# Kernel tuning notes

Measured on AMD Instinct MI355X. Metric: run time of the kernel, lower is better.

## Reference

```python
import jax, jax.numpy as jnp
import numpy as np

N_M, N_D, E = 20000, 8000, 200000
F_IN, H, O = 384, 512, 256  # feature dim, hidden_channels, out_channels
H1 = O * 2                  # conv1 output channels = 512


def setup_inputs() -> dict:
    key = jax.random.key(0)
    ks = jax.random.split(key, 32)

    def w(k, shape):
        return jax.random.normal(k, shape, dtype=jnp.float32) * 0.02

    inp = {
        # node features
        "mirna_feat": jax.random.normal(ks[0], (N_M, F_IN), dtype=jnp.float32),
        "dis_feat": jax.random.normal(ks[1], (N_D, F_IN), dtype=jnp.float32),
        # node ids and edge list (miRNA -> disease); reverse edges are the flip
        "mirna_node_id": jnp.arange(N_M, dtype=jnp.int32),
        "dis_node_id": jnp.arange(N_D, dtype=jnp.int32),
        "edge_src": jax.random.randint(ks[2], (E,), 0, N_M, dtype=jnp.int32),
        "edge_dst": jax.random.randint(ks[3], (E,), 0, N_D, dtype=jnp.int32),
        # input projections + embeddings
        "Wm": w(ks[4], (F_IN, H)), "bm": jnp.zeros((H,), jnp.float32),
        "Wd": w(ks[5], (F_IN, H)), "bd": jnp.zeros((H,), jnp.float32),
        "mirna_emb": w(ks[6], (N_M, H)),
        "dis_emb": w(ks[7], (N_D, H)),
        # layer1 SAGEConv per edge type (md: miRNA->disease, dm: reverse)
        "W1_md_l": w(ks[8], (H, H1)), "b1_md": jnp.zeros((H1,), jnp.float32), "W1_md_r": w(ks[9], (H, H1)),
        "W1_dm_l": w(ks[10], (H, H1)), "b1_dm": jnp.zeros((H1,), jnp.float32), "W1_dm_r": w(ks[11], (H, H1)),
        # layer2 SAGEConv per edge type
        "W2_md_l": w(ks[12], (H1, O)), "b2_md": jnp.zeros((O,), jnp.float32), "W2_md_r": w(ks[13], (H1, O)),
        "W2_dm_l": w(ks[14], (H1, O)), "b2_dm": jnp.zeros((O,), jnp.float32), "W2_dm_r": w(ks[15], (H1, O)),
    }
    return inp


def _mean_agg(x_src, src_idx, dst_idx, n_dst):
    # gather src features per edge, segment-mean onto destinations (0 for isolated nodes)
    msg = jnp.take(x_src, src_idx, axis=0)               # [E, d]
    agg = jax.ops.segment_sum(msg, dst_idx, num_segments=n_dst)
    cnt = jax.ops.segment_sum(jnp.ones((dst_idx.shape[0],), x_src.dtype), dst_idx, num_segments=n_dst)
    return agg / jnp.maximum(cnt, 1.0)[:, None]


def _sage(x_src, x_dst, src_idx, dst_idx, Wl, bl, Wr):
    mean = _mean_agg(x_src, src_idx, dst_idx, x_dst.shape[0])
    return mean @ Wl + bl + x_dst @ Wr


def reference(mirna_feat, dis_feat, mirna_node_id, dis_node_id, edge_src, edge_dst,
              Wm, bm, Wd, bd, mirna_emb, dis_emb,
              W1_md_l, b1_md, W1_md_r, W1_dm_l, b1_dm, W1_dm_r,
              W2_md_l, b2_md, W2_md_r, W2_dm_l, b2_dm, W2_dm_r):
    # input encoders
    x_m = mirna_feat @ Wm + bm + jnp.take(mirna_emb, mirna_node_id, axis=0)
    x_d = dis_feat @ Wd + bd + jnp.take(dis_emb, dis_node_id, axis=0)
    # hetero SAGE layer 1 (each dst type has exactly one incoming edge type)
    h_d = _sage(x_m, x_d, edge_src, edge_dst, W1_md_l, b1_md, W1_md_r)
    h_m = _sage(x_d, x_m, edge_dst, edge_src, W1_dm_l, b1_dm, W1_dm_r)
    h_m, h_d = jax.nn.relu(h_m), jax.nn.relu(h_d)
    # hetero SAGE layer 2
    o_d = _sage(h_m, h_d, edge_src, edge_dst, W2_md_l, b2_md, W2_md_r)
    o_m = _sage(h_d, h_m, edge_dst, edge_src, W2_dm_l, b2_dm, W2_dm_r)
    return (o_m, o_d)
```

## Files before the change

### kernel.cpp

```cpp
#include <hip/hip_runtime.h>

#define DEVI __device__ __forceinline__

typedef __attribute__((ext_vector_type(8))) short bf16x8;
typedef __attribute__((ext_vector_type(4))) float f32x4;

static constexpr int NM = 20000, ND = 8000, NE = 200000;
static constexpr int FIN = 384, H = 512, H1 = 512, O = 256;

DEVI float bf2f(unsigned int u){ union{unsigned int i; float f;}v; v.i=u<<16; return v.f; }
DEVI unsigned int f2bf(float f){ union{float f; unsigned int i;}v; v.f=f;
  return (v.i + 0x7FFFu + ((v.i>>16)&1u))>>16; }

DEVI void gload16(const void* g, void* l){
  __builtin_amdgcn_global_load_lds((const __attribute__((address_space(1))) unsigned int*)g,
                                   (__attribute__((address_space(3))) unsigned int*)l, 16, 0, 0);
}

template<int EPI>
__global__ __launch_bounds__(256)
void gemm_bf16(const unsigned short* __restrict__ A0,
               const unsigned short* __restrict__ A1, int KA,
               const unsigned short* __restrict__ WT, int Ktot,
               const float* __restrict__ bias,
               const float* __restrict__ emb, const int* __restrict__ ids,
               void* __restrict__ outp, int M, int N)
{
  __shared__ unsigned short sA[128*64];
  __shared__ unsigned short sB[128*64];
  const int tid  = threadIdx.x;
  const int lane = tid & 63;
  const int wv   = tid >> 6;
  const int wr   = wv >> 1, wc = wv & 1;
  const int bm0  = blockIdx.x * 128;
  const int bn0  = blockIdx.y * 128;

  f32x4 acc[4][4];
  #pragma unroll
  for (int m=0;m<4;++m)
    #pragma unroll
    for (int n=0;n<4;++n) acc[m][n] = (f32x4){0.f,0.f,0.f,0.f};

  const int r = tid >> 3;
  const int c = tid & 7;
  const int KT = Ktot >> 6;

  for (int kt = 0; kt < KT; ++kt) {
    const int kbase = kt << 6;
    const unsigned short* Ap; int ka, astr;
    if (kbase < KA) { Ap = A0; ka = kbase;      astr = KA; }
    else            { Ap = A1; ka = kbase - KA; astr = Ktot - KA; }
    #pragma unroll
    for (int it = 0; it < 4; ++it) {
      const int row = r + it*32;
      int grA = bm0 + row; grA = grA < M ? grA : M-1;
      const int cc = (c ^ (row & 7)) * 8;
      gload16(Ap + (size_t)grA*astr + ka + cc,    &sA[row*64 + c*8]);
      gload16(WT + (size_t)(bn0+row)*Ktot + kbase + cc, &sB[row*64 + c*8]);
    }
    __syncthreads();
    #pragma unroll
    for (int kk = 0; kk < 2; ++kk) {
      bf16x8 af[4], bfr[4];
      #pragma unroll
      for (int m=0;m<4;++m){
        const int rl = wr*64 + m*16 + (lane&15);
        const int ch = (kk*4 + (lane>>4)) ^ (rl&7);
        af[m] = *(const bf16x8*)&sA[rl*64 + ch*8];
      }
      #pragma unroll
      for (int n=0;n<4;++n){
        const int rl = wc*64 + n*16 + (lane&15);
        const int ch = (kk*4 + (lane>>4)) ^ (rl&7);
        bfr[n] = *(const bf16x8*)&sB[rl*64 + ch*8];
      }
      #pragma unroll
      for (int m=0;m<4;++m)
        #pragma unroll
        for (int n=0;n<4;++n)
          acc[m][n] = __builtin_amdgcn_mfma_f32_16x16x32_bf16(af[m], bfr[n], acc[m][n], 0,0,0);
    }
    __syncthreads();
  }

  const int cl = lane & 15;
  const int rg = lane >> 4;
  #pragma unroll
  for (int n=0;n<4;++n){
    const int col = bn0 + wc*64 + n*16 + cl;
    const float bv = bias[col];
    #pragma unroll
    for (int m=0;m<4;++m){
      const int rowb = bm0 + wr*64 + m*16 + rg*4;
      #pragma unroll
      for (int j=0;j<4;++j){
        const int row = rowb + j;
        if (row < M) {
          float v = acc[m][n][j] + bv;
          if constexpr (EPI==0) v += emb[(size_t)ids[row]*N + col];
          if constexpr (EPI==1) v = v > 0.f ? v : 0.f;
          if constexpr (EPI==2) ((float*)outp)[(size_t)row*N + col] = v;
          else ((unsigned short*)outp)[(size_t)row*N + col] = (unsigned short)f2bf(v);
        }
      }
    }
  }
}

__global__ __launch_bounds__(256)
void agg_mean(const unsigned short* __restrict__ X,
              const int* __restrict__ off, const int* __restrict__ nbr,
              unsigned short* __restrict__ out, int Nd)
{
  const int node = blockIdx.x*4 + (threadIdx.x>>6);
  if (node >= Nd) return;
  const int lane = threadIdx.x & 63;
  const int s = off[node], e = off[node+1];
  float a[8] = {0.f,0.f,0.f,0.f,0.f,0.f,0.f,0.f};
  for (int j = s; j < e; ++j){
    const int src = nbr[j];
    const uint4 v = *(const uint4*)(X + (size_t)src*H + lane*8);
    a[0]+=bf2f(v.x&0xffffu); a[1]+=bf2f(v.x>>16);
    a[2]+=bf2f(v.y&0xffffu); a[3]+=bf2f(v.y>>16);
    a[4]+=bf2f(v.z&0xffffu); a[5]+=bf2f(v.z>>16);
    a[6]+=bf2f(v.w&0xffffu); a[7]+=bf2f(v.w>>16);
  }
  const float inv = (e > s) ? 1.0f/(float)(e - s) : 0.0f;
  uint4 o;
  o.x = f2bf(a[0]*inv) | (f2bf(a[1]*inv)<<16);
  o.y = f2bf(a[2]*inv) | (f2bf(a[3]*inv)<<16);
  o.z = f2bf(a[4]*inv) | (f2bf(a[5]*inv)<<16);
  o.w = f2bf(a[6]*inv) | (f2bf(a[7]*inv)<<16);
  *(uint4*)(out + (size_t)node*H + lane*8) = o;
}

DEVI void tpart(int t, const float* __restrict__ in, unsigned short* __restrict__ out,
                int K, int N, int koff, int Kt)
{
  const int n = t / K, k = t - n*K;
  out[(size_t)n*Kt + koff + k] = (unsigned short)f2bf(in[(size_t)k*N + n]);
}

__global__ __launch_bounds__(256)
void prep_w(const float* Wm, const float* Wd,
            const float* W1mdl, const float* W1mdr, const float* W1dml, const float* W1dmr,
            const float* W2mdl, const float* W2mdr, const float* W2dml, const float* W2dmr,
            unsigned short* WmT, unsigned short* WdT,
            unsigned short* W1mdT, unsigned short* W1dmT,
            unsigned short* W2mdT, unsigned short* W2dmT)
{
  int t = blockIdx.x*256 + threadIdx.x;
  const int sE = FIN*H, s1 = H*H1, s2 = H1*O;
  if (t < sE){ tpart(t, Wm,    WmT,   FIN, H, 0,   FIN ); return; } t -= sE;
  if (t < sE){ tpart(t, Wd,    WdT,   FIN, H, 0,   FIN ); return; } t -= sE;
  if (t < s1){ tpart(t, W1mdl, W1mdT, H,  H1, 0,   1024); return; } t -= s1;
  if (t < s1){ tpart(t, W1mdr, W1mdT, H,  H1, 512, 1024); return; } t -= s1;
  if (t < s1){ tpart(t, W1dml, W1dmT, H,  H1, 0,   1024); return; } t -= s1;
  if (t < s1){ tpart(t, W1dmr, W1dmT, H,  H1, 512, 1024); return; } t -= s1;
  if (t < s2){ tpart(t, W2mdl, W2mdT, H1, O,  0,   1024); return; } t -= s2;
  if (t < s2){ tpart(t, W2mdr, W2mdT, H1, O,  512, 1024); return; } t -= s2;
  if (t < s2){ tpart(t, W2dml, W2dmT, H1, O,  0,   1024); return; } t -= s2;
  if (t < s2){ tpart(t, W2dmr, W2dmT, H1, O,  512, 1024); return; }
}

__global__ __launch_bounds__(256)
void cvt_feat(const float* __restrict__ fm, const float* __restrict__ fd,
              unsigned short* __restrict__ om, unsigned short* __restrict__ od)
{
  const long nm = (long)NM*FIN/4, nd = (long)ND*FIN/4;
  const long i = (long)blockIdx.x*256 + threadIdx.x;
  if (i >= nm+nd) return;
  const float4 v = (i < nm) ? ((const float4*)fm)[i] : ((const float4*)fd)[i-nm];
  uint2 o; o.x = f2bf(v.x) | (f2bf(v.y)<<16); o.y = f2bf(v.z) | (f2bf(v.w)<<16);
  if (i < nm) ((uint2*)om)[i] = o; else ((uint2*)od)[i-nm] = o;
}

__global__ __launch_bounds__(256)
void hist_k(const int* __restrict__ esrc, const int* __restrict__ edst,
            int* __restrict__ degm, int* __restrict__ degd)
{
  const int e = blockIdx.x*256 + threadIdx.x;
  if (e < NE){ atomicAdd(&degd[edst[e]], 1); atomicAdd(&degm[esrc[e]], 1); }
}

__global__ __launch_bounds__(256)
void scan_k(const int* __restrict__ degd, int* __restrict__ offd, int* __restrict__ curd,
            const int* __restrict__ degm, int* __restrict__ offm, int* __restrict__ curm)
{
  const int* deg; int* off; int* cur; int n;
  if (blockIdx.x == 0){ deg=degd; off=offd; cur=curd; n=ND; }
  else                { deg=degm; off=offm; cur=curm; n=NM; }
  __shared__ int ps[257];
  const int t = threadIdx.x;
  const int chunk = (n + 255) >> 8;
  int lo = t*chunk;     if (lo > n) lo = n;
  int hi = lo + chunk;  if (hi > n) hi = n;
  int s = 0;
  for (int i=lo;i<hi;++i) s += deg[i];
  ps[t+1] = s;
  if (t==0) ps[0] = 0;
  __syncthreads();
  if (t==0){ for (int i=1;i<=256;++i) ps[i] += ps[i-1]; }
  __syncthreads();
  int run = ps[t];
  for (int i=lo;i<hi;++i){ off[i]=run; cur[i]=run; run += deg[i]; }
  if (t==0) off[n] = ps[256];
}

__global__ __launch_bounds__(256)
void fill_k(const int* __restrict__ esrc, const int* __restrict__ edst,
            int* __restrict__ curd, int* __restrict__ curm,
            int* __restrict__ ebd, int* __restrict__ ebs)
{
  const int e = blockIdx.x*256 + threadIdx.x;
  if (e < NE){
    const int s = esrc[e], d = edst[e];
    ebd[atomicAdd(&curd[d],1)] = s;
    ebs[atomicAdd(&curm[s],1)] = d;
  }
}

extern "C" void kernel_launch(void* const* d_in, const int* in_sizes, int n_in,
                              void* d_out, int out_size, void* d_ws, size_t ws_size,
                              hipStream_t stream)
{
  (void)in_sizes; (void)n_in; (void)out_size; (void)ws_size;
  const float* mirna_feat=(const float*)d_in[0];
  const float* dis_feat  =(const float*)d_in[1];
  const int*   m_id =(const int*)d_in[2];
  const int*   d_id =(const int*)d_in[3];
  const int*   esrc =(const int*)d_in[4];
  const int*   edst =(const int*)d_in[5];
  const float* Wm=(const float*)d_in[6];  const float* bm=(const float*)d_in[7];
  const float* Wd=(const float*)d_in[8];  const float* bd=(const float*)d_in[9];
  const float* m_emb=(const float*)d_in[10]; const float* d_emb=(const float*)d_in[11];
  const float* W1mdl=(const float*)d_in[12]; const float* b1md=(const float*)d_in[13];
  const float* W1mdr=(const float*)d_in[14];
  const float* W1dml=(const float*)d_in[15]; const float* b1dm=(const float*)d_in[16];
  const float* W1dmr=(const float*)d_in[17];
  const float* W2mdl=(const float*)d_in[18]; const float* b2md=(const float*)d_in[19];
  const float* W2mdr=(const float*)d_in[20];
  const float* W2dml=(const float*)d_in[21]; const float* b2dm=(const float*)d_in[22];
  const float* W2dmr=(const float*)d_in[23];

  size_t off = 0;
  char* base = (char*)d_ws;
  auto alloc = [&](size_t bytes)->void*{
    off = (off + 255) & ~(size_t)255;
    void* p = base + off; off += bytes; return p;
  };
  unsigned short* featm = (unsigned short*)alloc((size_t)NM*FIN*2);
  unsigned short* featd = (unsigned short*)alloc((size_t)ND*FIN*2);
  unsigned short* WmT   = (unsigned short*)alloc((size_t)H*FIN*2);
  unsigned short* WdT   = (unsigned short*)alloc((size_t)H*FIN*2);
  unsigned short* W1mdT = (unsigned short*)alloc((size_t)H1*1024*2);
  unsigned short* W1dmT = (unsigned short*)alloc((size_t)H1*1024*2);
  unsigned short* W2mdT = (unsigned short*)alloc((size_t)O*1024*2);
  unsigned short* W2dmT = (unsigned short*)alloc((size_t)O*1024*2);
  unsigned short* xm    = (unsigned short*)alloc((size_t)NM*H*2);
  unsigned short* xd    = (unsigned short*)alloc((size_t)ND*H*2);
  unsigned short* aggm  = (unsigned short*)alloc((size_t)NM*H*2);
  unsigned short* aggd  = (unsigned short*)alloc((size_t)ND*H*2);
  unsigned short* hm    = (unsigned short*)alloc((size_t)NM*H1*2);
  unsigned short* hd    = (unsigned short*)alloc((size_t)ND*H1*2);
  int* degd = (int*)alloc((size_t)(ND+NM)*4);
  int* degm = degd + ND;
  int* offd = (int*)alloc((size_t)(ND+1)*4);
  int* offm = (int*)alloc((size_t)(NM+1)*4);
  int* curd = (int*)alloc((size_t)ND*4);
  int* curm = (int*)alloc((size_t)NM*4);
  int* ebd  = (int*)alloc((size_t)NE*4);
  int* ebs  = (int*)alloc((size_t)NE*4);

  hipMemsetAsync(degd, 0, (size_t)(ND+NM)*4, stream);
  prep_w<<<7680,256,0,stream>>>(Wm,Wd,W1mdl,W1mdr,W1dml,W1dmr,W2mdl,W2mdr,W2dml,W2dmr,
                                WmT,WdT,W1mdT,W1dmT,W2mdT,W2dmT);
  cvt_feat<<<10500,256,0,stream>>>(mirna_feat, dis_feat, featm, featd);
  hist_k<<<(NE+255)/256,256,0,stream>>>(esrc, edst, degm, degd);
  scan_k<<<2,256,0,stream>>>(degd, offd, curd, degm, offm, curm);
  fill_k<<<(NE+255)/256,256,0,stream>>>(esrc, edst, curd, curm, ebd, ebs);

  gemm_bf16<0><<<dim3(157,4),256,0,stream>>>(featm, featm, FIN, WmT, FIN, bm, m_emb, m_id, xm, NM, H);
  gemm_bf16<0><<<dim3( 63,4),256,0,stream>>>(featd, featd, FIN, WdT, FIN, bd, d_emb, d_id, xd, ND, H);
  agg_mean<<<ND/4,256,0,stream>>>(xm, offd, ebd, aggd, ND);
  agg_mean<<<NM/4,256,0,stream>>>(xd, offm, ebs, aggm, NM);
  gemm_bf16<1><<<dim3( 63,4),256,0,stream>>>(aggd, xd, H, W1mdT, 1024, b1md, nullptr, nullptr, hd, ND, H1);
  gemm_bf16<1><<<dim3(157,4),256,0,stream>>>(aggm, xm, H, W1dmT, 1024, b1dm, nullptr, nullptr, hm, NM, H1);
  agg_mean<<<ND/4,256,0,stream>>>(hm, offd, ebd, aggd, ND);
  agg_mean<<<NM/4,256,0,stream>>>(hd, offm, ebs, aggm, NM);
  float* out_m = (float*)d_out;
  float* out_d = out_m + (size_t)NM*O;
  gemm_bf16<2><<<dim3( 63,2),256,0,stream>>>(aggd, hd, H1, W2mdT, 1024, b2md, nullptr, nullptr, out_d, ND, O);
  gemm_bf16<2><<<dim3(157,2),256,0,stream>>>(aggm, hm, H1, W2dmT, 1024, b2dm, nullptr, nullptr, out_m, NM, O);
}
```

Measured before the change: 658.2 us.

## Double-buffer GEMM LDS tiles and merge paired GEMM, aggregation and prep launches

The GEMM kernel now double-buffers its LDS tiles, issuing async global-to-LDS loads for the next K tile while the MFMAs run on the current one. The miRNA and disease halves of each GEMM and each mean-aggregation are merged into single launches that pick their part by block index, and the three prep kernels are folded into one. The aim is to hide load latency and cut launch count and tail idle time between small kernels. Doubling LDS to 64KB per block may lower occupancy, and the read of the current buffer in the last k-step may race with the prefetch into the other buffer only if the barriers are misplaced.

```diff
diff --git a/kernel.cpp b/kernel.cpp
--- a/kernel.cpp
+++ b/kernel.cpp
@@ -17,23 +17,36 @@
                                    (__attribute__((address_space(3))) unsigned int*)l, 16, 0, 0);
 }
 
+struct GPart {
+  const unsigned short* A0;
+  const unsigned short* A1;
+  const unsigned short* WT;
+  const float* bias;
+  const float* emb;
+  const int* ids;
+  void* out;
+  int M;
+  int nbx;
+};
+
 template<int EPI>
 __global__ __launch_bounds__(256)
-void gemm_bf16(const unsigned short* __restrict__ A0,
-               const unsigned short* __restrict__ A1, int KA,
-               const unsigned short* __restrict__ WT, int Ktot,
-               const float* __restrict__ bias,
-               const float* __restrict__ emb, const int* __restrict__ ids,
-               void* __restrict__ outp, int M, int N)
-{
-  __shared__ unsigned short sA[128*64];
-  __shared__ unsigned short sB[128*64];
+void gemm2(GPart P0, GPart P1, int KA, int Ktot, int N)
+{
+  __shared__ unsigned short sA[2][128*64];
+  __shared__ unsigned short sB[2][128*64];
+
+  int bx = blockIdx.x;
+  const GPart& P = (bx < P0.nbx) ? P0 : P1;
+  if (bx >= P0.nbx) bx -= P0.nbx;
+
   const int tid  = threadIdx.x;
   const int lane = tid & 63;
   const int wv   = tid >> 6;
   const int wr   = wv >> 1, wc = wv & 1;
-  const int bm0  = blockIdx.x * 128;
+  const int bm0  = bx * 128;
   const int bn0  = blockIdx.y * 128;
+  const int M    = P.M;
 
   f32x4 acc[4][4];
   #pragma unroll
@@ -45,20 +58,26 @@
   const int c = tid & 7;
   const int KT = Ktot >> 6;
 
-  for (int kt = 0; kt < KT; ++kt) {
+  auto STAGE = [&](int buf, int kt){
     const int kbase = kt << 6;
     const unsigned short* Ap; int ka, astr;
-    if (kbase < KA) { Ap = A0; ka = kbase;      astr = KA; }
-    else            { Ap = A1; ka = kbase - KA; astr = Ktot - KA; }
+    if (kbase < KA) { Ap = P.A0; ka = kbase;      astr = KA; }
+    else            { Ap = P.A1; ka = kbase - KA; astr = Ktot - KA; }
     #pragma unroll
     for (int it = 0; it < 4; ++it) {
       const int row = r + it*32;
       int grA = bm0 + row; grA = grA < M ? grA : M-1;
       const int cc = (c ^ (row & 7)) * 8;
-      gload16(Ap + (size_t)grA*astr + ka + cc,    &sA[row*64 + c*8]);
-      gload16(WT + (size_t)(bn0+row)*Ktot + kbase + cc, &sB[row*64 + c*8]);
+      gload16(Ap   + (size_t)grA*astr      + ka    + cc, &sA[buf][row*64 + c*8]);
+      gload16(P.WT + (size_t)(bn0+row)*Ktot + kbase + cc, &sB[buf][row*64 + c*8]);
     }
-    __syncthreads();
+  };
+
+  STAGE(0, 0);
+  __syncthreads();
+  int cur = 0;
+  for (int kt = 0; kt < KT; ++kt) {
+    if (kt + 1 < KT) STAGE(cur ^ 1, kt + 1);
     #pragma unroll
     for (int kk = 0; kk < 2; ++kk) {
       bf16x8 af[4], bfr[4];
@@ -66,13 +85,13 @@
       for (int m=0;m<4;++m){
         const int rl = wr*64 + m*16 + (lane&15);
         const int ch = (kk*4 + (lane>>4)) ^ (rl&7);
-        af[m] = *(const bf16x8*)&sA[rl*64 + ch*8];
+        af[m] = *(const bf16x8*)&sA[cur][rl*64 + ch*8];
       }
       #pragma unroll
       for (int n=0;n<4;++n){
         const int rl = wc*64 + n*16 + (lane&15);
         const int ch = (kk*4 + (lane>>4)) ^ (rl&7);
-        bfr[n] = *(const bf16x8*)&sB[rl*64 + ch*8];
+        bfr[n] = *(const bf16x8*)&sB[cur][rl*64 + ch*8];
       }
       #pragma unroll
       for (int m=0;m<4;++m)
@@ -81,6 +100,7 @@
           acc[m][n] = __builtin_amdgcn_mfma_f32_16x16x32_bf16(af[m], bfr[n], acc[m][n], 0,0,0);
     }
     __syncthreads();
+    cur ^= 1;
   }
 
   const int cl = lane & 15;
@@ -88,7 +108,7 @@
   #pragma unroll
   for (int n=0;n<4;++n){
     const int col = bn0 + wc*64 + n*16 + cl;
-    const float bv = bias[col];
+    const float bv = P.bias[col];
     #pragma unroll
     for (int m=0;m<4;++m){
       const int rowb = bm0 + wr*64 + m*16 + rg*4;
@@ -97,10 +117,10 @@
         const int row = rowb + j;
         if (row < M) {
           float v = acc[m][n][j] + bv;
-          if constexpr (EPI==0) v += emb[(size_t)ids[row]*N + col];
+          if constexpr (EPI==0) v += P.emb[(size_t)P.ids[row]*N + col];
           if constexpr (EPI==1) v = v > 0.f ? v : 0.f;
-          if constexpr (EPI==2) ((float*)outp)[(size_t)row*N + col] = v;
-          else ((unsigned short*)outp)[(size_t)row*N + col] = (unsigned short)f2bf(v);
+          if constexpr (EPI==2) ((float*)P.out)[(size_t)row*N + col] = v;
+          else ((unsigned short*)P.out)[(size_t)row*N + col] = (unsigned short)f2bf(v);
         }
       }
     }
@@ -108,12 +128,15 @@
 }
 
 __global__ __launch_bounds__(256)
-void agg_mean(const unsigned short* __restrict__ X,
-              const int* __restrict__ off, const int* __restrict__ nbr,
-              unsigned short* __restrict__ out, int Nd)
-{
-  const int node = blockIdx.x*4 + (threadIdx.x>>6);
-  if (node >= Nd) return;
+void agg2(const unsigned short* __restrict__ Xm, const unsigned short* __restrict__ Xd,
+          const int* __restrict__ offm, const int* __restrict__ ebs,
+          const int* __restrict__ offd, const int* __restrict__ ebd,
+          unsigned short* __restrict__ aggm, unsigned short* __restrict__ aggd)
+{
+  int node = blockIdx.x*4 + (threadIdx.x>>6);
+  const unsigned short* X; const int* off; const int* nbr; unsigned short* out;
+  if (node < NM){ X = Xd; off = offm; nbr = ebs; out = aggm; }
+  else          { node -= NM; X = Xm; off = offd; nbr = ebd; out = aggd; }
   const int lane = threadIdx.x & 63;
   const int s = off[node], e = off[node+1];
   float a[8] = {0.f,0.f,0.f,0.f,0.f,0.f,0.f,0.f};
@@ -141,46 +164,45 @@
   out[(size_t)n*Kt + koff + k] = (unsigned short)f2bf(in[(size_t)k*N + n]);
 }
 
-__global__ __launch_bounds__(256)
-void prep_w(const float* Wm, const float* Wd,
-            const float* W1mdl, const float* W1mdr, const float* W1dml, const float* W1dmr,
-            const float* W2mdl, const float* W2mdr, const float* W2dml, const float* W2dmr,
-            unsigned short* WmT, unsigned short* WdT,
-            unsigned short* W1mdT, unsigned short* W1dmT,
-            unsigned short* W2mdT, unsigned short* W2dmT)
-{
-  int t = blockIdx.x*256 + threadIdx.x;
-  const int sE = FIN*H, s1 = H*H1, s2 = H1*O;
-  if (t < sE){ tpart(t, Wm,    WmT,   FIN, H, 0,   FIN ); return; } t -= sE;
-  if (t < sE){ tpart(t, Wd,    WdT,   FIN, H, 0,   FIN ); return; } t -= sE;
-  if (t < s1){ tpart(t, W1mdl, W1mdT, H,  H1, 0,   1024); return; } t -= s1;
-  if (t < s1){ tpart(t, W1mdr, W1mdT, H,  H1, 512, 1024); return; } t -= s1;
-  if (t < s1){ tpart(t, W1dml, W1dmT, H,  H1, 0,   1024); return; } t -= s1;
-  if (t < s1){ tpart(t, W1dmr, W1dmT, H,  H1, 512, 1024); return; } t -= s1;
-  if (t < s2){ tpart(t, W2mdl, W2mdT, H1, O,  0,   1024); return; } t -= s2;
-  if (t < s2){ tpart(t, W2mdr, W2mdT, H1, O,  512, 1024); return; } t -= s2;
-  if (t < s2){ tpart(t, W2dml, W2dmT, H1, O,  0,   1024); return; } t -= s2;
-  if (t < s2){ tpart(t, W2dmr, W2dmT, H1, O,  512, 1024); return; }
-}
-
-__global__ __launch_bounds__(256)
-void cvt_feat(const float* __restrict__ fm, const float* __restrict__ fd,
-              unsigned short* __restrict__ om, unsigned short* __restrict__ od)
-{
-  const long nm = (long)NM*FIN/4, nd = (long)ND*FIN/4;
-  const long i = (long)blockIdx.x*256 + threadIdx.x;
-  if (i >= nm+nd) return;
-  const float4 v = (i < nm) ? ((const float4*)fm)[i] : ((const float4*)fd)[i-nm];
-  uint2 o; o.x = f2bf(v.x) | (f2bf(v.y)<<16); o.y = f2bf(v.z) | (f2bf(v.w)<<16);
-  if (i < nm) ((uint2*)om)[i] = o; else ((uint2*)od)[i-nm] = o;
-}
-
-__global__ __launch_bounds__(256)
-void hist_k(const int* __restrict__ esrc, const int* __restrict__ edst,
-            int* __restrict__ degm, int* __restrict__ degd)
-{
-  const int e = blockIdx.x*256 + threadIdx.x;
-  if (e < NE){ atomicAdd(&degd[edst[e]], 1); atomicAdd(&degm[esrc[e]], 1); }
+static constexpr int PREPW_BLOCKS = 7680;
+static constexpr int CVT_BLOCKS   = 10500;
+static constexpr int HIST_BLOCKS  = (NE + 255)/256;
+
+__global__ __launch_bounds__(256)
+void prep_all(const float* Wm, const float* Wd,
+              const float* W1mdl, const float* W1mdr, const float* W1dml, const float* W1dmr,
+              const float* W2mdl, const float* W2mdr, const float* W2dml, const float* W2dmr,
+              unsigned short* WmT, unsigned short* WdT,
+              unsigned short* W1mdT, unsigned short* W1dmT,
+              unsigned short* W2mdT, unsigned short* W2dmT,
+              const float* fm, const float* fd, unsigned short* om, unsigned short* od,
+              const int* esrc, const int* edst, int* degm, int* degd)
+{
+  const int b = blockIdx.x;
+  if (b < PREPW_BLOCKS) {
+    int t = b*256 + threadIdx.x;
+    const int sE = FIN*H, s1 = H*H1, s2 = H1*O;
+    if (t < sE){ tpart(t, Wm,    WmT,   FIN, H, 0,   FIN ); return; } t -= sE;
+    if (t < sE){ tpart(t, Wd,    WdT,   FIN, H, 0,   FIN ); return; } t -= sE;
+    if (t < s1){ tpart(t, W1mdl, W1mdT, H,  H1, 0,   1024); return; } t -= s1;
+    if (t < s1){ tpart(t, W1mdr, W1mdT, H,  H1, 512, 1024); return; } t -= s1;
+    if (t < s1){ tpart(t, W1dml, W1dmT, H,  H1, 0,   1024); return; } t -= s1;
+    if (t < s1){ tpart(t, W1dmr, W1dmT, H,  H1, 512, 1024); return; } t -= s1;
+    if (t < s2){ tpart(t, W2mdl, W2mdT, H1, O,  0,   1024); return; } t -= s2;
+    if (t < s2){ tpart(t, W2mdr, W2mdT, H1, O,  512, 1024); return; } t -= s2;
+    if (t < s2){ tpart(t, W2dml, W2dmT, H1, O,  0,   1024); return; } t -= s2;
+    if (t < s2){ tpart(t, W2dmr, W2dmT, H1, O,  512, 1024); return; }
+  } else if (b < PREPW_BLOCKS + CVT_BLOCKS) {
+    const long nm = (long)NM*FIN/4, nd = (long)ND*FIN/4;
+    const long i = (long)(b - PREPW_BLOCKS)*256 + threadIdx.x;
+    if (i >= nm+nd) return;
+    const float4 v = (i < nm) ? ((const float4*)fm)[i] : ((const float4*)fd)[i-nm];
+    uint2 o; o.x = f2bf(v.x) | (f2bf(v.y)<<16); o.y = f2bf(v.z) | (f2bf(v.w)<<16);
+    if (i < nm) ((uint2*)om)[i] = o; else ((uint2*)od)[i-nm] = o;
+  } else {
+    const int e = (b - PREPW_BLOCKS - CVT_BLOCKS)*256 + threadIdx.x;
+    if (e < NE){ atomicAdd(&degd[edst[e]], 1); atomicAdd(&degm[esrc[e]], 1); }
+  }
 }
 
 __global__ __launch_bounds__(256)
@@ -273,23 +295,31 @@
   int* ebs  = (int*)alloc((size_t)NE*4);
 
   hipMemsetAsync(degd, 0, (size_t)(ND+NM)*4, stream);
-  prep_w<<<7680,256,0,stream>>>(Wm,Wd,W1mdl,W1mdr,W1dml,W1dmr,W2mdl,W2mdr,W2dml,W2dmr,
-                                WmT,WdT,W1mdT,W1dmT,W2mdT,W2dmT);
-  cvt_feat<<<10500,256,0,stream>>>(mirna_feat, dis_feat, featm, featd);
-  hist_k<<<(NE+255)/256,256,0,stream>>>(esrc, edst, degm, degd);
+  prep_all<<<PREPW_BLOCKS + CVT_BLOCKS + HIST_BLOCKS, 256, 0, stream>>>(
+      Wm,Wd,W1mdl,W1mdr,W1dml,W1dmr,W2mdl,W2mdr,W2dml,W2dmr,
+      WmT,WdT,W1mdT,W1dmT,W2mdT,W2dmT,
+      mirna_feat, dis_feat, featm, featd,
+      esrc, edst, degm, degd);
   scan_k<<<2,256,0,stream>>>(degd, offd, curd, degm, offm, curm);
   fill_k<<<(NE+255)/256,256,0,stream>>>(esrc, edst, curd, curm, ebd, ebs);
 
-  gemm_bf16<0><<<dim3(157,4),256,0,stream>>>(featm, featm, FIN, WmT, FIN, bm, m_emb, m_id, xm, NM, H);
-  gemm_bf16<0><<<dim3( 63,4),256,0,stream>>>(featd, featd, FIN, WdT, FIN, bd, d_emb, d_id, xd, ND, H);
-  agg_mean<<<ND/4,256,0,stream>>>(xm, offd, ebd, aggd, ND);
-  agg_mean<<<NM/4,256,0,stream>>>(xd, offm, ebs, aggm, NM);
-  gemm_bf16<1><<<dim3( 63,4),256,0,stream>>>(aggd, xd, H, W1mdT, 1024, b1md, nullptr, nullptr, hd, ND, H1);
-  gemm_bf16<1><<<dim3(157,4),256,0,stream>>>(aggm, xm, H, W1dmT, 1024, b1dm, nullptr, nullptr, hm, NM, H1);
-  agg_mean<<<ND/4,256,0,stream>>>(hm, offd, ebd, aggd, ND);
-  agg_mean<<<NM/4,256,0,stream>>>(hd, offm, ebs, aggm, NM);
+  {
+    GPart p0{featm, featm, WmT, bm, m_emb, m_id, xm, NM, 157};
+    GPart p1{featd, featd, WdT, bd, d_emb, d_id, xd, ND, 63};
+    gemm2<0><<<dim3(220,4),256,0,stream>>>(p0, p1, FIN, FIN, H);
+  }
+  agg2<<<(NM+ND)/4,256,0,stream>>>(xm, xd, offm, ebs, offd, ebd, aggm, aggd);
+  {
+    GPart p0{aggm, xm, W1dmT, b1dm, nullptr, nullptr, hm, NM, 157};
+    GPart p1{aggd, xd, W1mdT, b1md, nullptr, nullptr, hd, ND, 63};
+    gemm2<1><<<dim3(220,4),256,0,stream>>>(p0, p1, H, 1024, H1);
+  }
+  agg2<<<(NM+ND)/4,256,0,stream>>>(hm, hd, offm, ebs, offd, ebd, aggm, aggd);
   float* out_m = (float*)d_out;
   float* out_d = out_m + (size_t)NM*O;
-  gemm_bf16<2><<<dim3( 63,2),256,0,stream>>>(aggd, hd, H1, W2mdT, 1024, b2md, nullptr, nullptr, out_d, ND, O);
-  gemm_bf16<2><<<dim3(157,2),256,0,stream>>>(aggm, hm, H1, W2dmT, 1024, b2dm, nullptr, nullptr, out_m, NM, O);
-}
+  {
+    GPart p0{aggm, hm, W2dmT, b2dm, nullptr, nullptr, out_m, NM, 157};
+    GPart p1{aggd, hd, W2mdT, b2md, nullptr, nullptr, out_d, ND, 63};
+    gemm2<2><<<dim3(220,2),256,0,stream>>>(p0, p1, H1, 1024, O);
+  }
+}
```

Result: faster. 598.7 us (-9.1%).
